# Kernel optimization log

Measured on AMD Instinct MI355X. Metric: run time of the kernel, lower is better.

## Reference

```python
import jax, jax.numpy as jnp
import numpy as np

P = 4        # number of sequence pairs (half batch)
L = 512      # sequence length
D = 64       # embedding dim
NUM_CLASSES = 4
BIAS_INIT = 10.0


def setup_inputs() -> dict:
    key = jax.random.key(0)
    k1, k2, k3 = jax.random.split(key, 3)
    seqs_logits = jax.random.normal(k1, (2 * P, L, D), dtype=jnp.float32)
    ordinal_weight = jax.random.normal(k2, (1, NUM_CLASSES), dtype=jnp.float32)
    ordinal_bias = jax.random.normal(k3, (NUM_CLASSES,), dtype=jnp.float32) + BIAS_INIT
    return {"seqs_logits": seqs_logits, "ordinal_weight": ordinal_weight,
            "ordinal_bias": ordinal_bias}


def reference(seqs_logits, ordinal_weight, ordinal_bias):
    half = seqs_logits.shape[0] // 2
    z0 = seqs_logits[:half]          # [P, L0, D]
    z1 = seqs_logits[half:2 * half]  # [P, L1, D]

    def score_plus(z0_i, z1_i):
        # pairwise negative L1 distance: [L0, L1]
        s = -jnp.sum(jnp.abs(z0_i[:, None, :] - z1_i[None, :, :]), axis=-1)
        a = jax.nn.softmax(s, axis=1)   # row-wise alignment
        b = jax.nn.softmax(s, axis=0)   # column-wise alignment
        c = a + b - a * b               # symmetric soft alignment
        c_val = jnp.sum(c * s) / jnp.sum(c)
        logit = c_val * ordinal_weight + ordinal_bias  # [1, 4]
        return logit.reshape(-1)        # [4]

    return jax.vmap(score_plus)(z0, z1)  # [P, 4]
```

## Files before the change

### kernel.cpp

```cpp
#include <hip/hip_runtime.h>
#include <math.h>

#define P 4
#define L 512
#define D 64
#define NC 4
#define RS 68
#define SHIFT 64.0f

#define COLP_O 0
#define ROWP_O 16384
#define BP_O   32768
#define SV_O   33280

__global__ __launch_bounds__(256) void dist_stats(const float* __restrict__ z,
                                                  float* __restrict__ ws) {
    const int bx = blockIdx.x;
    const int pair = bx >> 6, kb = (bx >> 3) & 7, jb = bx & 7;
    const int tid = threadIdx.x, tx = tid & 15, ty = tid >> 4;
    const int wave = tid >> 6, lane = tid & 63;

    __shared__ float jt[64][RS], kt[64][RS];
    __shared__ float csred[4][64];

    {
        const float4* z0t = (const float4*)(z + ((size_t)pair * L + jb * 64) * D);
        const float4* z1t = (const float4*)(z + ((size_t)(P + pair) * L + kb * 64) * D);
        #pragma unroll
        for (int i = 0; i < 4; ++i) {
            const int li = i * 256 + tid;
            const float4 a = z0t[li];
            const float4 b = z1t[li];
            *(float4*)&jt[li >> 4][(li & 15) * 4] = a;
            *(float4*)&kt[li >> 4][(li & 15) * 4] = b;
        }
    }
    __syncthreads();

    float acc[4][4];
    #pragma unroll
    for (int r = 0; r < 4; ++r)
        #pragma unroll
        for (int q = 0; q < 4; ++q) acc[r][q] = 0.f;
    #pragma unroll
    for (int c = 0; c < 16; ++c) {
        float4 jv[4], kv[4];
        #pragma unroll
        for (int r = 0; r < 4; ++r) jv[r] = *(const float4*)&jt[ty + 16 * r][c * 4];
        #pragma unroll
        for (int q = 0; q < 4; ++q) kv[q] = *(const float4*)&kt[tx + 16 * q][c * 4];
        #pragma unroll
        for (int r = 0; r < 4; ++r)
            #pragma unroll
            for (int q = 0; q < 4; ++q)
                acc[r][q] += fabsf(jv[r].x - kv[q].x) + fabsf(jv[r].y - kv[q].y)
                           + fabsf(jv[r].z - kv[q].z) + fabsf(jv[r].w - kv[q].w);
    }

    {
        float* svb = ws + SV_O + (size_t)bx * 4096;
        #pragma unroll
        for (int r = 0; r < 4; ++r)
            #pragma unroll
            for (int q = 0; q < 4; ++q)
                svb[(r * 4 + q) * 256 + tid] = -acc[r][q];
    }

    float rs_[4] = {0.f, 0.f, 0.f, 0.f};
    float cs_[4] = {0.f, 0.f, 0.f, 0.f};
    #pragma unroll
    for (int r = 0; r < 4; ++r)
        #pragma unroll
        for (int q = 0; q < 4; ++q) {
            const float e = __expf(SHIFT - acc[r][q]);
            rs_[r] += e;
            cs_[q] += e;
        }
    #pragma unroll
    for (int off = 1; off <= 8; off <<= 1)
        #pragma unroll
        for (int r = 0; r < 4; ++r) rs_[r] += __shfl_xor(rs_[r], off);
    if (tx == 0) {
        #pragma unroll
        for (int r = 0; r < 4; ++r)
            ws[ROWP_O + (pair * 8 + kb) * 512 + jb * 64 + ty + 16 * r] = rs_[r];
    }
    #pragma unroll
    for (int off = 16; off <= 32; off <<= 1)
        #pragma unroll
        for (int q = 0; q < 4; ++q) cs_[q] += __shfl_xor(cs_[q], off);
    if ((lane >> 4) == 0) {
        #pragma unroll
        for (int q = 0; q < 4; ++q) csred[wave][q * 16 + tx] = cs_[q];
    }
    __syncthreads();
    if (tid < 64)
        ws[COLP_O + (pair * 8 + jb) * 512 + kb * 64 + (tid & 15) + 16 * (tid >> 4)]
            = csred[0][tid] + csred[1][tid] + csred[2][tid] + csred[3][tid];
}

__global__ __launch_bounds__(256) void c_accum(const float* __restrict__ wsc,
                                               float* __restrict__ ws) {
    const int bx = blockIdx.x;
    const int pair = bx >> 6, kb = (bx >> 3) & 7, jb = bx & 7;
    const int tid = threadIdx.x, tx = tid & 15, ty = tid >> 4;
    const int wave = tid >> 6, lane = tid & 63;

    __shared__ float rtmp[64][4], ctmp[64][4];
    __shared__ float rrcp_s[64], crcp_s[64];
    __shared__ float bred[4][2];

    {
        const int l = tid >> 2, p4 = tid & 3;
        rtmp[l][p4] = wsc[ROWP_O + (pair * 8 + 2 * p4) * 512 + jb * 64 + l]
                    + wsc[ROWP_O + (pair * 8 + 2 * p4 + 1) * 512 + jb * 64 + l];
        ctmp[l][p4] = wsc[COLP_O + (pair * 8 + 2 * p4) * 512 + kb * 64 + l]
                    + wsc[COLP_O + (pair * 8 + 2 * p4 + 1) * 512 + kb * 64 + l];
    }
    __syncthreads();
    if (tid < 64) {
        rrcp_s[tid] = 1.0f / (rtmp[tid][0] + rtmp[tid][1] + rtmp[tid][2] + rtmp[tid][3]);
    } else if (tid < 128) {
        const int l = tid - 64;
        crcp_s[l] = 1.0f / (ctmp[l][0] + ctmp[l][1] + ctmp[l][2] + ctmp[l][3]);
    }
    __syncthreads();

    const float* svb = wsc + SV_O + (size_t)bx * 4096;
    float cs = 0.f, cc = 0.f;
    #pragma unroll
    for (int r = 0; r < 4; ++r) {
        const float rr = rrcp_s[ty + 16 * r];
        #pragma unroll
        for (int q = 0; q < 4; ++q) {
            const float cr = crcp_s[tx + 16 * q];
            const float sv = svb[(r * 4 + q) * 256 + tid];
            const float e  = __expf(SHIFT + sv);
            const float a  = e * rr;
            const float b  = e * cr;
            const float c  = a + b - a * b;
            cs += c * sv;
            cc += c;
        }
    }
    #pragma unroll
    for (int off = 1; off <= 32; off <<= 1) {
        cs += __shfl_xor(cs, off);
        cc += __shfl_xor(cc, off);
    }
    if (lane == 0) { bred[wave][0] = cs; bred[wave][1] = cc; }
    __syncthreads();
    if (tid == 0) {
        const int bidp = kb * 8 + jb;
        ws[BP_O + (pair * 64 + bidp) * 2]     = bred[0][0] + bred[1][0] + bred[2][0] + bred[3][0];
        ws[BP_O + (pair * 64 + bidp) * 2 + 1] = bred[0][1] + bred[1][1] + bred[2][1] + bred[3][1];
    }
}

__global__ __launch_bounds__(256) void finalize(const float* __restrict__ ws,
                                                const float* __restrict__ w,
                                                const float* __restrict__ bias,
                                                float* __restrict__ out) {
    const int tid = threadIdx.x;
    const int pair = tid >> 6, lane = tid & 63;
    float cs = ws[BP_O + (pair * 64 + lane) * 2];
    float cc = ws[BP_O + (pair * 64 + lane) * 2 + 1];
    #pragma unroll
    for (int off = 1; off <= 32; off <<= 1) {
        cs += __shfl_xor(cs, off);
        cc += __shfl_xor(cc, off);
    }
    if (lane == 0) {
        const float c_val = cs / cc;
        #pragma unroll
        for (int cls = 0; cls < NC; ++cls)
            out[pair * NC + cls] = c_val * w[cls] + bias[cls];
    }
}

extern "C" void kernel_launch(void* const* d_in, const int* in_sizes, int n_in,
                              void* d_out, int out_size, void* d_ws, size_t ws_size,
                              hipStream_t stream) {
    const float* z    = (const float*)d_in[0];
    const float* w    = (const float*)d_in[1];
    const float* bias = (const float*)d_in[2];
    float* out = (float*)d_out;
    float* ws  = (float*)d_ws;

    dist_stats<<<dim3(P * 64), dim3(256), 0, stream>>>(z, ws);
    c_accum   <<<dim3(P * 64), dim3(256), 0, stream>>>(ws, ws);
    finalize  <<<dim3(1),      dim3(256), 0, stream>>>(ws, w, bias, out);
}
```

Measured before the change: 68.34 us.

## Fuse three kernels into one persistent kernel with grid barriers

Merges the distance/statistics, alignment-accumulate and finalize kernels into one launch of 256 blocks, separated by atomic-counter grid barriers. The distance tile now stays in registers across the barrier, so the per-block score matrix is no longer written to and re-read from global workspace. This removes two kernel launch gaps and that global round trip. In exchange it adds a memset launch to reset the barrier counter, plus spin-wait barrier cost. It also depends on all 256 blocks being resident at the same time.

```diff
diff --git a/kernel.cpp b/kernel.cpp
--- a/kernel.cpp
+++ b/kernel.cpp
@@ -11,17 +11,38 @@
 #define COLP_O 0
 #define ROWP_O 16384
 #define BP_O   32768
-#define SV_O   33280
+#define BAR_O  33280
 
-__global__ __launch_bounds__(256) void dist_stats(const float* __restrict__ z,
-                                                  float* __restrict__ ws) {
+#define NBLK 256
+
+__device__ __forceinline__ void grid_bar(unsigned* bar, unsigned goal) {
+    __syncthreads();
+    __threadfence();
+    if (threadIdx.x == 0) {
+        atomicAdd(bar, 1u);
+        while (__hip_atomic_load(bar, __ATOMIC_RELAXED, __HIP_MEMORY_SCOPE_AGENT) < goal)
+            __builtin_amdgcn_s_sleep(2);
+    }
+    __syncthreads();
+    __threadfence();
+}
+
+__global__ __launch_bounds__(256) void ssa_fused(const float* __restrict__ z,
+                                                 const float* __restrict__ w,
+                                                 const float* __restrict__ bias,
+                                                 float* __restrict__ out,
+                                                 float* __restrict__ ws) {
     const int bx = blockIdx.x;
     const int pair = bx >> 6, kb = (bx >> 3) & 7, jb = bx & 7;
     const int tid = threadIdx.x, tx = tid & 15, ty = tid >> 4;
     const int wave = tid >> 6, lane = tid & 63;
+    unsigned* bar = (unsigned*)(ws + BAR_O);
 
     __shared__ float jt[64][RS], kt[64][RS];
     __shared__ float csred[4][64];
+    __shared__ float rtmp[64][4], ctmp[64][4];
+    __shared__ float rrcp_s[64], crcp_s[64];
+    __shared__ float bred[4][2];
 
     {
         const float4* z0t = (const float4*)(z + ((size_t)pair * L + jb * 64) * D);
@@ -58,64 +79,47 @@
     }
 
     {
-        float* svb = ws + SV_O + (size_t)bx * 4096;
+        float rs_[4] = {0.f, 0.f, 0.f, 0.f};
+        float cs_[4] = {0.f, 0.f, 0.f, 0.f};
         #pragma unroll
         for (int r = 0; r < 4; ++r)
             #pragma unroll
-            for (int q = 0; q < 4; ++q)
-                svb[(r * 4 + q) * 256 + tid] = -acc[r][q];
+            for (int q = 0; q < 4; ++q) {
+                const float e = __expf(SHIFT - acc[r][q]);
+                rs_[r] += e;
+                cs_[q] += e;
+            }
+        #pragma unroll
+        for (int off = 1; off <= 8; off <<= 1)
+            #pragma unroll
+            for (int r = 0; r < 4; ++r) rs_[r] += __shfl_xor(rs_[r], off);
+        if (tx == 0) {
+            #pragma unroll
+            for (int r = 0; r < 4; ++r)
+                ws[ROWP_O + (pair * 8 + kb) * 512 + jb * 64 + ty + 16 * r] = rs_[r];
+        }
+        #pragma unroll
+        for (int off = 16; off <= 32; off <<= 1)
+            #pragma unroll
+            for (int q = 0; q < 4; ++q) cs_[q] += __shfl_xor(cs_[q], off);
+        if ((lane >> 4) == 0) {
+            #pragma unroll
+            for (int q = 0; q < 4; ++q) csred[wave][q * 16 + tx] = cs_[q];
+        }
+        __syncthreads();
+        if (tid < 64)
+            ws[COLP_O + (pair * 8 + jb) * 512 + kb * 64 + (tid & 15) + 16 * (tid >> 4)]
+                = csred[0][tid] + csred[1][tid] + csred[2][tid] + csred[3][tid];
     }
 
-    float rs_[4] = {0.f, 0.f, 0.f, 0.f};
-    float cs_[4] = {0.f, 0.f, 0.f, 0.f};
-    #pragma unroll
-    for (int r = 0; r < 4; ++r)
-        #pragma unroll
-        for (int q = 0; q < 4; ++q) {
-            const float e = __expf(SHIFT - acc[r][q]);
-            rs_[r] += e;
-            cs_[q] += e;
-        }
-    #pragma unroll
-    for (int off = 1; off <= 8; off <<= 1)
-        #pragma unroll
-        for (int r = 0; r < 4; ++r) rs_[r] += __shfl_xor(rs_[r], off);
-    if (tx == 0) {
-        #pragma unroll
-        for (int r = 0; r < 4; ++r)
-            ws[ROWP_O + (pair * 8 + kb) * 512 + jb * 64 + ty + 16 * r] = rs_[r];
-    }
-    #pragma unroll
-    for (int off = 16; off <= 32; off <<= 1)
-        #pragma unroll
-        for (int q = 0; q < 4; ++q) cs_[q] += __shfl_xor(cs_[q], off);
-    if ((lane >> 4) == 0) {
-        #pragma unroll
-        for (int q = 0; q < 4; ++q) csred[wave][q * 16 + tx] = cs_[q];
-    }
-    __syncthreads();
-    if (tid < 64)
-        ws[COLP_O + (pair * 8 + jb) * 512 + kb * 64 + (tid & 15) + 16 * (tid >> 4)]
-            = csred[0][tid] + csred[1][tid] + csred[2][tid] + csred[3][tid];
-}
-
-__global__ __launch_bounds__(256) void c_accum(const float* __restrict__ wsc,
-                                               float* __restrict__ ws) {
-    const int bx = blockIdx.x;
-    const int pair = bx >> 6, kb = (bx >> 3) & 7, jb = bx & 7;
-    const int tid = threadIdx.x, tx = tid & 15, ty = tid >> 4;
-    const int wave = tid >> 6, lane = tid & 63;
-
-    __shared__ float rtmp[64][4], ctmp[64][4];
-    __shared__ float rrcp_s[64], crcp_s[64];
-    __shared__ float bred[4][2];
+    grid_bar(bar, NBLK);
 
     {
         const int l = tid >> 2, p4 = tid & 3;
-        rtmp[l][p4] = wsc[ROWP_O + (pair * 8 + 2 * p4) * 512 + jb * 64 + l]
-                    + wsc[ROWP_O + (pair * 8 + 2 * p4 + 1) * 512 + jb * 64 + l];
-        ctmp[l][p4] = wsc[COLP_O + (pair * 8 + 2 * p4) * 512 + kb * 64 + l]
-                    + wsc[COLP_O + (pair * 8 + 2 * p4 + 1) * 512 + kb * 64 + l];
+        rtmp[l][p4] = ws[ROWP_O + (pair * 8 + 2 * p4) * 512 + jb * 64 + l]
+                    + ws[ROWP_O + (pair * 8 + 2 * p4 + 1) * 512 + jb * 64 + l];
+        ctmp[l][p4] = ws[COLP_O + (pair * 8 + 2 * p4) * 512 + kb * 64 + l]
+                    + ws[COLP_O + (pair * 8 + 2 * p4 + 1) * 512 + kb * 64 + l];
     }
     __syncthreads();
     if (tid < 64) {
@@ -126,55 +130,54 @@
     }
     __syncthreads();
 
-    const float* svb = wsc + SV_O + (size_t)bx * 4096;
-    float cs = 0.f, cc = 0.f;
-    #pragma unroll
-    for (int r = 0; r < 4; ++r) {
-        const float rr = rrcp_s[ty + 16 * r];
+    {
+        float cs = 0.f, cc = 0.f;
         #pragma unroll
-        for (int q = 0; q < 4; ++q) {
-            const float cr = crcp_s[tx + 16 * q];
-            const float sv = svb[(r * 4 + q) * 256 + tid];
-            const float e  = __expf(SHIFT + sv);
-            const float a  = e * rr;
-            const float b  = e * cr;
-            const float c  = a + b - a * b;
-            cs += c * sv;
-            cc += c;
+        for (int r = 0; r < 4; ++r) {
+            const float rr = rrcp_s[ty + 16 * r];
+            #pragma unroll
+            for (int q = 0; q < 4; ++q) {
+                const float cr = crcp_s[tx + 16 * q];
+                const float sv = -acc[r][q];
+                const float e  = __expf(SHIFT + sv);
+                const float a  = e * rr;
+                const float b  = e * cr;
+                const float c  = a + b - a * b;
+                cs += c * sv;
+                cc += c;
+            }
+        }
+        #pragma unroll
+        for (int off = 1; off <= 32; off <<= 1) {
+            cs += __shfl_xor(cs, off);
+            cc += __shfl_xor(cc, off);
+        }
+        if (lane == 0) { bred[wave][0] = cs; bred[wave][1] = cc; }
+        __syncthreads();
+        if (tid == 0) {
+            const int bidp = kb * 8 + jb;
+            ws[BP_O + (pair * 64 + bidp) * 2]     = bred[0][0] + bred[1][0] + bred[2][0] + bred[3][0];
+            ws[BP_O + (pair * 64 + bidp) * 2 + 1] = bred[0][1] + bred[1][1] + bred[2][1] + bred[3][1];
         }
     }
-    #pragma unroll
-    for (int off = 1; off <= 32; off <<= 1) {
-        cs += __shfl_xor(cs, off);
-        cc += __shfl_xor(cc, off);
-    }
-    if (lane == 0) { bred[wave][0] = cs; bred[wave][1] = cc; }
-    __syncthreads();
-    if (tid == 0) {
-        const int bidp = kb * 8 + jb;
-        ws[BP_O + (pair * 64 + bidp) * 2]     = bred[0][0] + bred[1][0] + bred[2][0] + bred[3][0];
-        ws[BP_O + (pair * 64 + bidp) * 2 + 1] = bred[0][1] + bred[1][1] + bred[2][1] + bred[3][1];
-    }
-}
 
-__global__ __launch_bounds__(256) void finalize(const float* __restrict__ ws,
-                                                const float* __restrict__ w,
-                                                const float* __restrict__ bias,
-                                                float* __restrict__ out) {
-    const int tid = threadIdx.x;
-    const int pair = tid >> 6, lane = tid & 63;
-    float cs = ws[BP_O + (pair * 64 + lane) * 2];
-    float cc = ws[BP_O + (pair * 64 + lane) * 2 + 1];
-    #pragma unroll
-    for (int off = 1; off <= 32; off <<= 1) {
-        cs += __shfl_xor(cs, off);
-        cc += __shfl_xor(cc, off);
-    }
-    if (lane == 0) {
-        const float c_val = cs / cc;
+    grid_bar(bar, 2 * NBLK);
+
+    if (bx == 0) {
+        const int p2 = tid >> 6, l2 = tid & 63;
+        float fcs = ws[BP_O + (p2 * 64 + l2) * 2];
+        float fcc = ws[BP_O + (p2 * 64 + l2) * 2 + 1];
         #pragma unroll
-        for (int cls = 0; cls < NC; ++cls)
-            out[pair * NC + cls] = c_val * w[cls] + bias[cls];
+        for (int off = 1; off <= 32; off <<= 1) {
+            fcs += __shfl_xor(fcs, off);
+            fcc += __shfl_xor(fcc, off);
+        }
+        if (l2 == 0) {
+            const float c_val = fcs / fcc;
+            #pragma unroll
+            for (int cls = 0; cls < NC; ++cls)
+                out[p2 * NC + cls] = c_val * w[cls] + bias[cls];
+        }
     }
 }
 
@@ -187,7 +190,7 @@
     float* out = (float*)d_out;
     float* ws  = (float*)d_ws;
 
-    dist_stats<<<dim3(P * 64), dim3(256), 0, stream>>>(z, ws);
-    c_accum   <<<dim3(P * 64), dim3(256), 0, stream>>>(ws, ws);
-    finalize  <<<dim3(1),      dim3(256), 0, stream>>>(ws, w, bias, out);
+    hipMemsetAsync((char*)d_ws + (size_t)BAR_O * sizeof(float), 0, 256, stream);
+
+    ssa_fused<<<dim3(NBLK), dim3(256), 0, stream>>>(z, w, bias, out, ws);
 }
```

Result: slower. 141.6 us (+107.2%).

## Recompute distances in second pass and fuse finalize via last-block atomic

Applied to the files above, without the earlier changes.

The second kernel no longer reads the pairwise distance matrix from workspace; it restages the input tiles and recomputes the L1 distances, so the first kernel skips writing 4 MB of scores. The separate finalize launch is folded into the second kernel: each block publishes its partial sums, bumps an atomic counter, and the last block does the final reduction. This trades extra compute (a second distance sweep) for less global memory traffic and one fewer launch, and it relies on the counter being reset by the first kernel.

```diff
diff --git a/kernel.cpp b/kernel.cpp
--- a/kernel.cpp
+++ b/kernel.cpp
@@ -11,7 +11,46 @@
 #define COLP_O 0
 #define ROWP_O 16384
 #define BP_O   32768
-#define SV_O   33280
+#define DONE_O 33280
+
+#define NBLK 256
+
+__device__ __forceinline__ void stage_tiles(const float* __restrict__ z,
+                                            int pair, int jb, int kb, int tid,
+                                            float (*jt)[RS], float (*kt)[RS]) {
+    const float4* z0t = (const float4*)(z + ((size_t)pair * L + jb * 64) * D);
+    const float4* z1t = (const float4*)(z + ((size_t)(P + pair) * L + kb * 64) * D);
+    #pragma unroll
+    for (int i = 0; i < 4; ++i) {
+        const int li = i * 256 + tid;
+        const float4 a = z0t[li];
+        const float4 b = z1t[li];
+        *(float4*)&jt[li >> 4][(li & 15) * 4] = a;
+        *(float4*)&kt[li >> 4][(li & 15) * 4] = b;
+    }
+}
+
+__device__ __forceinline__ void dist_sweep(const float (*jt)[RS], const float (*kt)[RS],
+                                           int tx, int ty, float acc[4][4]) {
+    #pragma unroll
+    for (int r = 0; r < 4; ++r)
+        #pragma unroll
+        for (int q = 0; q < 4; ++q) acc[r][q] = 0.f;
+    #pragma unroll
+    for (int c = 0; c < 16; ++c) {
+        float4 jv[4], kv[4];
+        #pragma unroll
+        for (int r = 0; r < 4; ++r) jv[r] = *(const float4*)&jt[ty + 16 * r][c * 4];
+        #pragma unroll
+        for (int q = 0; q < 4; ++q) kv[q] = *(const float4*)&kt[tx + 16 * q][c * 4];
+        #pragma unroll
+        for (int r = 0; r < 4; ++r)
+            #pragma unroll
+            for (int q = 0; q < 4; ++q)
+                acc[r][q] += fabsf(jv[r].x - kv[q].x) + fabsf(jv[r].y - kv[q].y)
+                           + fabsf(jv[r].z - kv[q].z) + fabsf(jv[r].w - kv[q].w);
+    }
+}
 
 __global__ __launch_bounds__(256) void dist_stats(const float* __restrict__ z,
                                                   float* __restrict__ ws) {
@@ -23,48 +62,13 @@
     __shared__ float jt[64][RS], kt[64][RS];
     __shared__ float csred[4][64];
 
-    {
-        const float4* z0t = (const float4*)(z + ((size_t)pair * L + jb * 64) * D);
-        const float4* z1t = (const float4*)(z + ((size_t)(P + pair) * L + kb * 64) * D);
-        #pragma unroll
-        for (int i = 0; i < 4; ++i) {
-            const int li = i * 256 + tid;
-            const float4 a = z0t[li];
-            const float4 b = z1t[li];
-            *(float4*)&jt[li >> 4][(li & 15) * 4] = a;
-            *(float4*)&kt[li >> 4][(li & 15) * 4] = b;
-        }
-    }
+    if (bx == 0 && tid == 0) *(unsigned*)&ws[DONE_O] = 0u;
+
+    stage_tiles(z, pair, jb, kb, tid, jt, kt);
     __syncthreads();
 
     float acc[4][4];
-    #pragma unroll
-    for (int r = 0; r < 4; ++r)
-        #pragma unroll
-        for (int q = 0; q < 4; ++q) acc[r][q] = 0.f;
-    #pragma unroll
-    for (int c = 0; c < 16; ++c) {
-        float4 jv[4], kv[4];
-        #pragma unroll
-        for (int r = 0; r < 4; ++r) jv[r] = *(const float4*)&jt[ty + 16 * r][c * 4];
-        #pragma unroll
-        for (int q = 0; q < 4; ++q) kv[q] = *(const float4*)&kt[tx + 16 * q][c * 4];
-        #pragma unroll
-        for (int r = 0; r < 4; ++r)
-            #pragma unroll
-            for (int q = 0; q < 4; ++q)
-                acc[r][q] += fabsf(jv[r].x - kv[q].x) + fabsf(jv[r].y - kv[q].y)
-                           + fabsf(jv[r].z - kv[q].z) + fabsf(jv[r].w - kv[q].w);
-    }
-
-    {
-        float* svb = ws + SV_O + (size_t)bx * 4096;
-        #pragma unroll
-        for (int r = 0; r < 4; ++r)
-            #pragma unroll
-            for (int q = 0; q < 4; ++q)
-                svb[(r * 4 + q) * 256 + tid] = -acc[r][q];
-    }
+    dist_sweep(jt, kt, tx, ty, acc);
 
     float rs_[4] = {0.f, 0.f, 0.f, 0.f};
     float cs_[4] = {0.f, 0.f, 0.f, 0.f};
@@ -99,17 +103,24 @@
             = csred[0][tid] + csred[1][tid] + csred[2][tid] + csred[3][tid];
 }
 
-__global__ __launch_bounds__(256) void c_accum(const float* __restrict__ wsc,
-                                               float* __restrict__ ws) {
+__global__ __launch_bounds__(256) void c_accum_fin(const float* __restrict__ z,
+                                                   const float* __restrict__ wsc,
+                                                   float* __restrict__ ws,
+                                                   const float* __restrict__ w,
+                                                   const float* __restrict__ bias,
+                                                   float* __restrict__ out) {
     const int bx = blockIdx.x;
     const int pair = bx >> 6, kb = (bx >> 3) & 7, jb = bx & 7;
     const int tid = threadIdx.x, tx = tid & 15, ty = tid >> 4;
     const int wave = tid >> 6, lane = tid & 63;
 
+    __shared__ float jt[64][RS], kt[64][RS];
     __shared__ float rtmp[64][4], ctmp[64][4];
     __shared__ float rrcp_s[64], crcp_s[64];
     __shared__ float bred[4][2];
-
+    __shared__ int lastflag;
+
+    stage_tiles(z, pair, jb, kb, tid, jt, kt);
     {
         const int l = tid >> 2, p4 = tid & 3;
         rtmp[l][p4] = wsc[ROWP_O + (pair * 8 + 2 * p4) * 512 + jb * 64 + l]
@@ -124,9 +135,11 @@
         const int l = tid - 64;
         crcp_s[l] = 1.0f / (ctmp[l][0] + ctmp[l][1] + ctmp[l][2] + ctmp[l][3]);
     }
-    __syncthreads();
-
-    const float* svb = wsc + SV_O + (size_t)bx * 4096;
+
+    float acc[4][4];
+    dist_sweep(jt, kt, tx, ty, acc);
+    __syncthreads();
+
     float cs = 0.f, cc = 0.f;
     #pragma unroll
     for (int r = 0; r < 4; ++r) {
@@ -134,7 +147,7 @@
         #pragma unroll
         for (int q = 0; q < 4; ++q) {
             const float cr = crcp_s[tx + 16 * q];
-            const float sv = svb[(r * 4 + q) * 256 + tid];
+            const float sv = -acc[r][q];
             const float e  = __expf(SHIFT + sv);
             const float a  = e * rr;
             const float b  = e * cr;
@@ -150,31 +163,32 @@
     }
     if (lane == 0) { bred[wave][0] = cs; bred[wave][1] = cc; }
     __syncthreads();
+
     if (tid == 0) {
-        const int bidp = kb * 8 + jb;
-        ws[BP_O + (pair * 64 + bidp) * 2]     = bred[0][0] + bred[1][0] + bred[2][0] + bred[3][0];
-        ws[BP_O + (pair * 64 + bidp) * 2 + 1] = bred[0][1] + bred[1][1] + bred[2][1] + bred[3][1];
-    }
-}
-
-__global__ __launch_bounds__(256) void finalize(const float* __restrict__ ws,
-                                                const float* __restrict__ w,
-                                                const float* __restrict__ bias,
-                                                float* __restrict__ out) {
-    const int tid = threadIdx.x;
-    const int pair = tid >> 6, lane = tid & 63;
-    float cs = ws[BP_O + (pair * 64 + lane) * 2];
-    float cc = ws[BP_O + (pair * 64 + lane) * 2 + 1];
-    #pragma unroll
-    for (int off = 1; off <= 32; off <<= 1) {
-        cs += __shfl_xor(cs, off);
-        cc += __shfl_xor(cc, off);
-    }
-    if (lane == 0) {
-        const float c_val = cs / cc;
-        #pragma unroll
-        for (int cls = 0; cls < NC; ++cls)
-            out[pair * NC + cls] = c_val * w[cls] + bias[cls];
+        const float bcs = bred[0][0] + bred[1][0] + bred[2][0] + bred[3][0];
+        const float bcc = bred[0][1] + bred[1][1] + bred[2][1] + bred[3][1];
+        __hip_atomic_store(&ws[BP_O + bx * 2],     bcs, __ATOMIC_RELAXED, __HIP_MEMORY_SCOPE_AGENT);
+        __hip_atomic_store(&ws[BP_O + bx * 2 + 1], bcc, __ATOMIC_RELAXED, __HIP_MEMORY_SCOPE_AGENT);
+        const unsigned old = __hip_atomic_fetch_add((unsigned*)&ws[DONE_O], 1u,
+                                                    __ATOMIC_ACQ_REL, __HIP_MEMORY_SCOPE_AGENT);
+        lastflag = (old == NBLK - 1);
+    }
+    __syncthreads();
+
+    if (lastflag) {
+        float fcs = __hip_atomic_load(&ws[BP_O + tid * 2],     __ATOMIC_RELAXED, __HIP_MEMORY_SCOPE_AGENT);
+        float fcc = __hip_atomic_load(&ws[BP_O + tid * 2 + 1], __ATOMIC_RELAXED, __HIP_MEMORY_SCOPE_AGENT);
+        #pragma unroll
+        for (int off = 1; off <= 32; off <<= 1) {
+            fcs += __shfl_xor(fcs, off);
+            fcc += __shfl_xor(fcc, off);
+        }
+        if (lane == 0) {
+            const float c_val = fcs / fcc;
+            #pragma unroll
+            for (int cls = 0; cls < NC; ++cls)
+                out[wave * NC + cls] = c_val * w[cls] + bias[cls];
+        }
     }
 }
 
@@ -187,7 +201,6 @@
     float* out = (float*)d_out;
     float* ws  = (float*)d_ws;
 
-    dist_stats<<<dim3(P * 64), dim3(256), 0, stream>>>(z, ws);
-    c_accum   <<<dim3(P * 64), dim3(256), 0, stream>>>(ws, ws);
-    finalize  <<<dim3(1),      dim3(256), 0, stream>>>(ws, w, bias, out);
-}
+    dist_stats <<<dim3(NBLK), dim3(256), 0, stream>>>(z, ws);
+    c_accum_fin<<<dim3(NBLK), dim3(256), 0, stream>>>(z, ws, ws, w, bias, out);
+}
```

Measured after the change: 80.21 us. 17.4% more time.
